# Performance work log

Hardware: AMD Instinct MI355X
Metric: run time of the kernel (lower is better)

Reference implementation:

```python
import jax, jax.numpy as jnp
import numpy as np

LOCAL_HEADS = 8
GLOBAL_HEADS = 4
HEAD_DIM = 16  # dim // local_heads


def setup_inputs() -> dict:
    key = jax.random.key(0)
    ks = jax.random.split(key, 6)
    B, N, C = 8, 1024, 128
    gdim = HEAD_DIM * GLOBAL_HEADS  # 64
    return {
        "x": jax.random.normal(ks[0], (B, N, C), dtype=jnp.float32),
        "masks": jax.random.uniform(ks[1], (N, N, 3), dtype=jnp.float32),
        "Wq": jax.random.normal(ks[2], (gdim, C), dtype=jnp.float32) * 0.05,
        "Wk": jax.random.normal(ks[3], (gdim, C), dtype=jnp.float32) * 0.05,
        "Wv": jax.random.normal(ks[4], (C, C), dtype=jnp.float32) * 0.05,
        "mask_proj": jax.random.normal(ks[5], (3, GLOBAL_HEADS * LOCAL_HEADS), dtype=jnp.float32),
    }


def reference(x, masks, Wq, Wk, Wv, mask_proj):
    B, N, C = x.shape
    # projections (torch Linear: y = x @ W.T)
    q = (x @ Wq.T).reshape(B, N, GLOBAL_HEADS, HEAD_DIM)   # [B,N,G,hd]
    k = (x @ Wk.T).reshape(B, N, GLOBAL_HEADS, HEAD_DIM)
    v = (x @ Wv.T).reshape(B, N, LOCAL_HEADS, HEAD_DIM)    # [B,N,L,hd]
    # raw global-head scores: [B,G,N,N]  (no 1/sqrt(d) scaling in original)
    attn = jnp.einsum('bigd,bjgd->bgij', q, k)
    # learned mask mixing: masks [N,N,3] @ mask_proj [3, G*L] -> [N,N,G,L]
    mw = (masks @ mask_proj).reshape(N, N, GLOBAL_HEADS, LOCAL_HEADS)
    # mix global heads into local heads: [B,L,N,N]
    scores = jnp.einsum('bgij,ijgl->blij', attn, mw)
    probs = jax.nn.softmax(scores, axis=-1)               # over keys j
    out = jnp.einsum('blij,bjld->bild', probs, v)         # [B,N,L,hd]
    return out.reshape(B, N, C)
```

## Files before the change

### kernel.cpp

```cpp
#include <hip/hip_runtime.h>

#define BB 8
#define NN 1024
#define CC 128
#define GG 4
#define LL 8
#define GD 64

typedef __attribute__((ext_vector_type(8))) short short8;
typedef __attribute__((ext_vector_type(4))) short short4v;
typedef __attribute__((ext_vector_type(4))) float floatx4;

__device__ __forceinline__ short f2b(float f) {
  union { float f; unsigned u; } c; c.f = f;
  unsigned u = c.u;
  return (short)((u + 0x7FFFu + ((u >> 16) & 1u)) >> 16);
}
__device__ __forceinline__ float b2f(short s) {
  union { unsigned u; float f; } c; c.u = ((unsigned)(unsigned short)s) << 16;
  return c.f;
}
__device__ __forceinline__ void split2(float v, short& hi, short& lo) {
  short h = f2b(v);
  hi = h;
  lo = f2b(v - b2f(h));
}

#if __has_builtin(__builtin_amdgcn_cvt_pk_bf16_f32)
__device__ __forceinline__ unsigned pk2(float a, float b) {
  auto r = __builtin_amdgcn_cvt_pk_bf16_f32(a, b);
  unsigned u; __builtin_memcpy(&u, &r, 4); return u;
}
#else
__device__ __forceinline__ unsigned pk2(float a, float b) {
  return (unsigned)(unsigned short)f2b(a) | ((unsigned)(unsigned short)f2b(b) << 16);
}
#endif

#if __has_builtin(__builtin_amdgcn_exp2f)
#define EXP2(x) __builtin_amdgcn_exp2f(x)
#else
#define EXP2(x) exp2f(x)
#endif

#define BHP 136

__global__ __launch_bounds__(256) void proj_kernel(
    const float* __restrict__ x, const float* __restrict__ Wq,
    const float* __restrict__ Wk, const float* __restrict__ Wv,
    short* __restrict__ qb, short* __restrict__ kb, short* __restrict__ vtb)
{
  __shared__ short bh[64 * BHP];
  __shared__ short bl[64 * BHP];
  const int t = threadIdx.x;
  const int nt = blockIdx.x & 3;
  const int mt = blockIdx.x >> 2;
  const int w = t >> 6;
  const int lane = t & 63;
  const int ln = lane & 15;
  const int hq = lane >> 4;
  const int arow = mt * 64 + w * 16 + ln;

  const float* wbase = (nt == 0) ? Wq : (nt == 1) ? Wk : (Wv + (nt - 2) * 64 * 128);

  {
    int r = t >> 2, c0 = (t & 3) * 32;
    const float* src = wbase + r * 128 + c0;
    #pragma unroll
    for (int z8 = 0; z8 < 4; ++z8) {
      float4 u0 = *(const float4*)(src + z8 * 8);
      float4 u1 = *(const float4*)(src + z8 * 8 + 4);
      float uv[8] = {u0.x,u0.y,u0.z,u0.w,u1.x,u1.y,u1.z,u1.w};
      union { short s[8]; short8 v; } H, L;
      #pragma unroll
      for (int z = 0; z < 8; ++z) split2(uv[z], H.s[z], L.s[z]);
      *(short8*)(bh + r * BHP + c0 + z8 * 8) = H.v;
      *(short8*)(bl + r * BHP + c0 + z8 * 8) = L.v;
    }
  }
  __syncthreads();

  const floatx4 zf = {0.f, 0.f, 0.f, 0.f};
  floatx4 acc[4] = {zf, zf, zf, zf};

  #pragma unroll
  for (int kc = 0; kc < 4; ++kc) {
    const float* xp = x + (long)arow * 128 + kc * 32 + hq * 8;
    float4 a0 = *(const float4*)xp;
    float4 a1 = *(const float4*)(xp + 4);
    union { short s[8]; short8 v; } Ah, Al;
    float av[8] = {a0.x,a0.y,a0.z,a0.w,a1.x,a1.y,a1.z,a1.w};
    #pragma unroll
    for (int z = 0; z < 8; ++z) split2(av[z], Ah.s[z], Al.s[z]);
    #pragma unroll
    for (int ns = 0; ns < 4; ++ns) {
      short8 Bh = *(const short8*)(bh + (ns * 16 + ln) * BHP + kc * 32 + hq * 8);
      short8 Bl = *(const short8*)(bl + (ns * 16 + ln) * BHP + kc * 32 + hq * 8);
      acc[ns] = __builtin_amdgcn_mfma_f32_16x16x32_bf16(Ah.v, Bh, acc[ns], 0,0,0);
      acc[ns] = __builtin_amdgcn_mfma_f32_16x16x32_bf16(Al.v, Bh, acc[ns], 0,0,0);
      acc[ns] = __builtin_amdgcn_mfma_f32_16x16x32_bf16(Ah.v, Bl, acc[ns], 0,0,0);
    }
  }

  if (nt < 2) {
    short* dst = (nt == 0) ? qb : kb;
    #pragma unroll
    for (int ns = 0; ns < 4; ++ns) {
      int col = ns * 16 + ln;
      #pragma unroll
      for (int reg = 0; reg < 4; ++reg) {
        int row = mt * 64 + w * 16 + hq * 4 + reg;
        dst[(long)row * 64 + col] = f2b(acc[ns][reg]);
      }
    }
  } else {
    int b = mt >> 4;
    int tok = (mt * 64 + w * 16 + hq * 4) & 1023;
    #pragma unroll
    for (int ns = 0; ns < 4; ++ns) {
      int cv = (nt - 2) * 64 + ns * 16 + ln;
      union { short s[4]; short4v v; } o;
      #pragma unroll
      for (int reg = 0; reg < 4; ++reg) o.s[reg] = f2b(acc[ns][reg]);
      *(short4v*)(vtb + ((long)b * CC + cv) * NN + tok) = o.v;
    }
  }
}

#define IT 16
#define JT 64
#define SPLIT 4
#define JSPAN 256
#define NTL 4
#define ARP 260
#define MRP 196

__global__ __launch_bounds__(256, 3) void attn_kernel(
    const short* __restrict__ qb, const short* __restrict__ kb,
    const short* __restrict__ vtb, const float* __restrict__ masks,
    const float* __restrict__ mask_proj,
    float* __restrict__ pnum, float* __restrict__ pden3)
{
  __shared__ float arec[IT * ARP];
  __shared__ float mrec[2][IT * MRP];

  const int t = threadIdx.x;
  const int sp = blockIdx.x & 3;
  const int itile = (blockIdx.x >> 2) & 63;
  const int b = blockIdx.x >> 8;
  const int i0 = itile * IT;

  const int w = t >> 6;
  const int lane = t & 63;
  const int ln = lane & 15;
  const int hq = lane >> 4;
  const int l0 = 2 * w, l1 = 2 * w + 1;

  short8 qf;
  {
    union { short s[8]; short8 v; } qq;
    #pragma unroll
    for (int z = 0; z < 8; ++z) qq.s[z] = 0;
    if (hq < 2)
      qq.v = *(const short8*)(qb + ((long)(b * NN + i0 + ln)) * GD + w * 16 + hq * 8);
    qf = qq.v;
  }
  const float LOG2E = 1.44269504088896340736f;
  float ycA[3][4], ycB[3][4];
  #pragma unroll
  for (int m = 0; m < 3; ++m)
    #pragma unroll
    for (int g = 0; g < 4; ++g) {
      ycA[m][g] = mask_proj[m * 32 + g * 8 + l0] * LOG2E;
      ycB[m][g] = mask_proj[m * 32 + g * 8 + l1] * LOG2E;
    }

  const floatx4 zf = {0.f, 0.f, 0.f, 0.f};
  floatx4 pv0 = zf, pv1 = zf;
  float den0 = 0.f, den1 = 0.f;

  const short* kbase = kb + (long)b * NN * GD;
  const short* v0base = vtb + ((long)b * CC + l0 * 16 + ln) * NN;
  const short* v1base = vtb + ((long)b * CC + l1 * 16 + ln) * NN;

  for (int jt = 0; jt < NTL; ++jt) {
    const int j0 = sp * JSPAN + jt * JT;
    float* mrp = mrec[jt & 1];

    #pragma unroll
    for (int it2 = 0; it2 < 3; ++it2) {
      int f = t + it2 * 256;
      int ii = f / 48;
      int rem = f - ii * 48;
      *(float4*)(mrp + ii * MRP + rem * 4) =
        *(const float4*)(masks + (long)(i0 + ii) * (NN * 3) + (long)j0 * 3 + rem * 4);
    }
    __syncthreads();

    #pragma unroll
    for (int jsub = 0; jsub < 4; ++jsub) {
      union { short s[8]; short8 v; } kk;
      #pragma unroll
      for (int z = 0; z < 8; ++z) kk.s[z] = 0;
      if (hq < 2)
        kk.v = *(const short8*)(kbase + (long)(j0 + jsub * 16 + ln) * GD + w * 16 + hq * 8);
      floatx4 at = __builtin_amdgcn_mfma_f32_16x16x32_bf16(qf, kk.v, zf, 0, 0, 0);
      float* ab = arec + (jsub * 16 + ln) * 4 + w;
      #pragma unroll
      for (int reg = 0; reg < 4; ++reg)
        ab[(hq * 4 + reg) * ARP] = at[reg];
    }
    __syncthreads();

    #pragma unroll
    for (int mf = 0; mf < 2; ++mf) {
      float mku[24];
      {
        const float* mb = mrp + ln * MRP + mf * 96 + hq * 24;
        #pragma unroll
        for (int q4 = 0; q4 < 6; ++q4)
          *(float4*)(mku + q4 * 4) = *(const float4*)(mb + q4 * 4);
      }
      short8 vf0 = *(const short8*)(v0base + j0 + mf * 32 + hq * 8);
      short8 vf1 = *(const short8*)(v1base + j0 + mf * 32 + hq * 8);
      const float* arA = arec + ln * ARP + (mf * 32 + hq * 8) * 4;
      union { unsigned u[4]; short8 v; } p0, p1;
      #pragma unroll
      for (int zp = 0; zp < 4; ++zp) {
        float eA[2], eB[2];
        #pragma unroll
        for (int zz = 0; zz < 2; ++zz) {
          int z = zp * 2 + zz;
          floatx4 a4 = *(const floatx4*)(arA + z * 4);
          float m0 = mku[z * 3], m1 = mku[z * 3 + 1], m2 = mku[z * 3 + 2];
          float wA0 = m0*ycA[0][0] + m1*ycA[1][0] + m2*ycA[2][0];
          float wA1 = m0*ycA[0][1] + m1*ycA[1][1] + m2*ycA[2][1];
          float wA2 = m0*ycA[0][2] + m1*ycA[1][2] + m2*ycA[2][2];
          float wA3 = m0*ycA[0][3] + m1*ycA[1][3] + m2*ycA[2][3];
          float wB0 = m0*ycB[0][0] + m1*ycB[1][0] + m2*ycB[2][0];
          float wB1 = m0*ycB[0][1] + m1*ycB[1][1] + m2*ycB[2][1];
          float wB2 = m0*ycB[0][2] + m1*ycB[1][2] + m2*ycB[2][2];
          float wB3 = m0*ycB[0][3] + m1*ycB[1][3] + m2*ycB[2][3];
          float sA = a4[0]*wA0 + a4[1]*wA1 + a4[2]*wA2 + a4[3]*wA3;
          float sB = a4[0]*wB0 + a4[1]*wB1 + a4[2]*wB2 + a4[3]*wB3;
          eA[zz] = EXP2(sA);
          eB[zz] = EXP2(sB);
        }
        den0 += eA[0] + eA[1];
        den1 += eB[0] + eB[1];
        p0.u[zp] = pk2(eA[0], eA[1]);
        p1.u[zp] = pk2(eB[0], eB[1]);
      }
      pv0 = __builtin_amdgcn_mfma_f32_16x16x32_bf16(p0.v, vf0, pv0, 0, 0, 0);
      pv1 = __builtin_amdgcn_mfma_f32_16x16x32_bf16(p1.v, vf1, pv1, 0, 0, 0);
    }
  }

  #pragma unroll
  for (int reg = 0; reg < 4; ++reg) {
    long row = ((long)(sp * BB + b)) * NN + i0 + hq * 4 + reg;
    pnum[row * CC + l0 * 16 + ln] = pv0[reg];
    pnum[row * CC + l1 * 16 + ln] = pv1[reg];
  }
  long drow = ((long)(sp * BB + b)) * NN + i0 + ln;
  pden3[drow * 32 + l0 * 4 + hq] = den0;
  pden3[drow * 32 + l1 * 4 + hq] = den1;
}

__global__ __launch_bounds__(256) void reduce_kernel(
    const float* __restrict__ pnum, const float* __restrict__ pden3,
    float* __restrict__ out)
{
  int e4 = blockIdx.x * 256 + threadIdx.x;
  int bi = e4 >> 5;
  int l = (e4 & 31) >> 2;
  const float4* p4 = (const float4*)pnum;
  float4 n = {0.f, 0.f, 0.f, 0.f};
  float den = 0.f;
  #pragma unroll
  for (int s = 0; s < SPLIT; ++s) {
    float4 ns = p4[e4 + (long)s * (BB * NN * CC / 4)];
    n.x += ns.x; n.y += ns.y; n.z += ns.z; n.w += ns.w;
    float4 d4 = *(const float4*)(pden3 + ((long)s * BB * NN + bi) * 32 + l * 4);
    den += d4.x + d4.y + d4.z + d4.w;
  }
  float inv = 1.0f / den;
  float4 o;
  o.x = n.x * inv; o.y = n.y * inv; o.z = n.z * inv; o.w = n.w * inv;
  ((float4*)out)[e4] = o;
}

extern "C" void kernel_launch(void* const* d_in, const int* in_sizes, int n_in,
                              void* d_out, int out_size, void* d_ws, size_t ws_size,
                              hipStream_t stream) {
  const float* x         = (const float*)d_in[0];
  const float* masks     = (const float*)d_in[1];
  const float* Wq        = (const float*)d_in[2];
  const float* Wk        = (const float*)d_in[3];
  const float* Wv        = (const float*)d_in[4];
  const float* mask_proj = (const float*)d_in[5];
  float* out = (float*)d_out;

  char* wsB = (char*)d_ws;
  short* qb    = (short*)(wsB);
  short* kb    = (short*)(wsB + (1l << 20));
  short* vtb   = (short*)(wsB + (2l << 20));
  float* pnum  = (float*)(wsB + (4l << 20));
  float* pden3 = (float*)(wsB + (20l << 20));

  proj_kernel<<<512, 256, 0, stream>>>(x, Wq, Wk, Wv, qb, kb, vtb);
  attn_kernel<<<BB * (NN / IT) * SPLIT, 256, 0, stream>>>(qb, kb, vtb, masks,
                                                          mask_proj, pnum, pden3);
  reduce_kernel<<<(BB * NN * CC / 4) / 256, 256, 0, stream>>>(pnum, pden3, out);
}
```

Before: 134.3 us.

## Halve key split and prefetch mask tiles through registers

Reduces the key-dimension split from four to two so each block covers twice as many key tiles, halving the partial numerator/denominator buffers written and reduced. Mask tiles are now loaded into registers one tile ahead and stored to a single shared buffer after the compute phase, replacing the double-buffered direct global-to-shared load. This aims to hide mask load latency and cut partial-sum traffic, at the cost of fewer blocks, an extra barrier per tile, and a possible wave-quantization tail.

```diff
diff --git a/kernel.cpp b/kernel.cpp
--- a/kernel.cpp
+++ b/kernel.cpp
@@ -129,9 +129,9 @@
 
 #define IT 16
 #define JT 64
-#define SPLIT 4
-#define JSPAN 256
-#define NTL 4
+#define SPLIT 2
+#define JSPAN 512
+#define NTL 8
 #define ARP 260
 #define MRP 196
 
@@ -142,12 +142,12 @@
     float* __restrict__ pnum, float* __restrict__ pden3)
 {
   __shared__ float arec[IT * ARP];
-  __shared__ float mrec[2][IT * MRP];
+  __shared__ float mrec[IT * MRP];
 
   const int t = threadIdx.x;
-  const int sp = blockIdx.x & 3;
-  const int itile = (blockIdx.x >> 2) & 63;
-  const int b = blockIdx.x >> 8;
+  const int sp = blockIdx.x & 1;
+  const int itile = (blockIdx.x >> 1) & 63;
+  const int b = blockIdx.x >> 7;
   const int i0 = itile * IT;
 
   const int w = t >> 6;
@@ -156,6 +156,17 @@
   const int hq = lane >> 4;
   const int l0 = 2 * w, l1 = 2 * w + 1;
 
+  const float* mgp[3];
+  float* mlp[3];
+  #pragma unroll
+  for (int it2 = 0; it2 < 3; ++it2) {
+    int f = t + it2 * 256;
+    int ii = f / 48;
+    int rem = f - ii * 48;
+    mgp[it2] = masks + (long)(i0 + ii) * (NN * 3) + rem * 4;
+    mlp[it2] = mrec + ii * MRP + rem * 4;
+  }
+
   short8 qf;
   {
     union { short s[8]; short8 v; } qq;
@@ -183,19 +194,18 @@
   const short* v0base = vtb + ((long)b * CC + l0 * 16 + ln) * NN;
   const short* v1base = vtb + ((long)b * CC + l1 * 16 + ln) * NN;
 
+  const int jb0 = sp * JSPAN;
+  float4 mpre[3];
+
+  #pragma unroll
+  for (int it2 = 0; it2 < 3; ++it2)
+    mpre[it2] = *(const float4*)(mgp[it2] + (long)jb0 * 3);
+  #pragma unroll
+  for (int it2 = 0; it2 < 3; ++it2)
+    *(float4*)(mlp[it2]) = mpre[it2];
+
   for (int jt = 0; jt < NTL; ++jt) {
-    const int j0 = sp * JSPAN + jt * JT;
-    float* mrp = mrec[jt & 1];
-
-    #pragma unroll
-    for (int it2 = 0; it2 < 3; ++it2) {
-      int f = t + it2 * 256;
-      int ii = f / 48;
-      int rem = f - ii * 48;
-      *(float4*)(mrp + ii * MRP + rem * 4) =
-        *(const float4*)(masks + (long)(i0 + ii) * (NN * 3) + (long)j0 * 3 + rem * 4);
-    }
-    __syncthreads();
+    const int j0 = jb0 + jt * JT;
 
     #pragma unroll
     for (int jsub = 0; jsub < 4; ++jsub) {
@@ -210,13 +220,20 @@
       for (int reg = 0; reg < 4; ++reg)
         ab[(hq * 4 + reg) * ARP] = at[reg];
     }
+
+    {
+      const long jn3 = (long)(jt + 1 < NTL ? j0 + JT : j0) * 3;
+      #pragma unroll
+      for (int it2 = 0; it2 < 3; ++it2)
+        mpre[it2] = *(const float4*)(mgp[it2] + jn3);
+    }
     __syncthreads();
 
     #pragma unroll
     for (int mf = 0; mf < 2; ++mf) {
       float mku[24];
       {
-        const float* mb = mrp + ln * MRP + mf * 96 + hq * 24;
+        const float* mb = mrec + ln * MRP + mf * 96 + hq * 24;
         #pragma unroll
         for (int q4 = 0; q4 < 6; ++q4)
           *(float4*)(mku + q4 * 4) = *(const float4*)(mb + q4 * 4);
@@ -254,6 +271,11 @@
       pv0 = __builtin_amdgcn_mfma_f32_16x16x32_bf16(p0.v, vf0, pv0, 0, 0, 0);
       pv1 = __builtin_amdgcn_mfma_f32_16x16x32_bf16(p1.v, vf1, pv1, 0, 0, 0);
     }
+    __syncthreads();
+
+    #pragma unroll
+    for (int it2 = 0; it2 < 3; ++it2)
+      *(float4*)(mlp[it2]) = mpre[it2];
   }
 
   #pragma unroll
@@ -306,7 +328,7 @@
   short* kb    = (short*)(wsB + (1l << 20));
   short* vtb   = (short*)(wsB + (2l << 20));
   float* pnum  = (float*)(wsB + (4l << 20));
-  float* pden3 = (float*)(wsB + (20l << 20));
+  float* pden3 = (float*)(wsB + (12l << 20));
 
   proj_kernel<<<512, 256, 0, stream>>>(x, Wq, Wk, Wv, qb, kb, vtb);
   attn_kernel<<<BB * (NN / IT) * SPLIT, 256, 0, stream>>>(qb, kb, vtb, masks,
```

Result: slower. 144.0 us (+7.3%).
